# Optimization experiments

Measured on AMD Instinct MI355X. Metric: run time of the kernel, lower is better.

The kernel has to match this reference:

```python
import jax, jax.numpy as jnp
import numpy as np

B, N, E, H, A = 64, 64, 4032, 256, 4  # batch, max atoms, edges per mol, hidden, edge-attr dim
FI = 2 * H + 1 + A  # edge-MLP input dim = 517
SCALE = 15.0


def setup_inputs() -> dict:
    key = jax.random.key(0)
    ks = jax.random.split(key, 16)
    w = lambda k, s: jax.random.normal(k, s, jnp.float32) * 0.05
    # edge indices with i != j to avoid degenerate zero-distance edges
    ii = jax.random.randint(ks[3], (B, E), 0, N)
    off = jax.random.randint(ks[4], (B, E), 1, N)
    jj = (ii + off) % N
    edge_indices = jnp.stack([ii, jj], axis=-1).astype(jnp.int32)
    return dict(
        x=jax.random.normal(ks[0], (B, N, 3), jnp.float32),
        h=jax.random.normal(ks[1], (B, N, H), jnp.float32),
        a=jax.random.normal(ks[2], (B, E, A), jnp.float32),
        edge_indices=edge_indices,
        node_mask=jnp.ones((B, N, 1), jnp.float32),
        edge_mask=jnp.ones((B, E, 1), jnp.float32),
        We1=w(ks[5], (FI, 256)), be1=jnp.zeros(256, jnp.float32),
        We2=w(ks[6], (256, 256)), be2=jnp.zeros(256, jnp.float32),
        Wa=w(ks[7], (256, 1)), ba=jnp.zeros(1, jnp.float32),
        Wh1=w(ks[8], (H + 256, 256)), bh1=jnp.zeros(256, jnp.float32),
        Wh2=w(ks[9], (256, 256)), bh2=jnp.zeros(256, jnp.float32),
        Wx1=w(ks[10], (FI, 256)), bx1=jnp.zeros(256, jnp.float32),
        Wx2=w(ks[11], (256, 256)), bx2=jnp.zeros(256, jnp.float32),
        Wx3=w(ks[12], (256, 1)),
    )


def reference(x, h, a, edge_indices, node_mask, edge_mask,
              We1, be1, We2, be2, Wa, ba,
              Wh1, bh1, Wh2, bh2, Wx1, bx1, Wx2, bx2, Wx3):
    silu = jax.nn.silu
    bidx = jnp.arange(B)[:, None]                      # [B,1] batch gather index
    ii, jj = edge_indices[..., 0], edge_indices[..., 1]
    x_i, x_j = x[bidx, ii], x[bidx, jj]                # [B,E,3]
    diff = (x_i - x_j) * edge_mask                     # [B,E,3]
    d = jnp.sqrt(jnp.sum(diff * diff, -1, keepdims=True))  # [B,E,1]
    h_i, h_j = h[bidx, ii], h[bidx, jj]                # [B,E,H]
    feat = jnp.concatenate([h_i, h_j, d * d, a], -1)   # [B,E,517]
    # edge MLP + attention gate
    m = silu(silu(feat @ We1 + be1) @ We2 + be2)       # [B,E,256]
    e = jax.nn.sigmoid(m @ Wa + ba)                    # [B,E,1]
    em = e * m
    # scatter-add to source nodes (replaces the one-hot matmul, same math)
    seg = (bidx * N + ii).reshape(-1)                  # [B*E]
    em_agg = jax.ops.segment_sum(em.reshape(B * E, 256), seg,
                                 num_segments=B * N).reshape(B, N, 256)
    h_out = (h + silu(jnp.concatenate([h, em_agg], -1) @ Wh1 + bh1) @ Wh2 + bh2) * node_mask
    # coordinate update
    xw = jnp.tanh(silu(silu(feat @ Wx1 + bx1) @ Wx2 + bx2) @ Wx3) * SCALE  # [B,E,1]
    xm = xw * diff / (d + 1.0)                         # [B,E,3]
    x_agg = jax.ops.segment_sum(xm.reshape(B * E, 3), seg,
                                num_segments=B * N).reshape(B, N, 3)
    x_out = (x + x_agg) * node_mask
    return x_out, h_out
```

## Files before the change

kernel.cpp:

```cpp
#include <hip/hip_runtime.h>

#define E_ 4032
#define TE 64
#define NB 4032

typedef unsigned int uint;
typedef unsigned short ushort;
typedef __attribute__((ext_vector_type(8))) short short8;
typedef __attribute__((ext_vector_type(4))) float f32x4;
typedef __attribute__((ext_vector_type(2))) float f32x2;

__device__ __forceinline__ ushort f2bf(float x) {
  uint u = __float_as_uint(x);
  return (ushort)((u + 0x7fffu + ((u >> 16) & 1u)) >> 16);
}
__device__ __forceinline__ uint pack2(float lo, float hi) {
  return (uint)f2bf(lo) | ((uint)f2bf(hi) << 16);
}
__device__ __forceinline__ uint cvtpk(float lo, float hi) {
  uint r;
  asm("v_cvt_pk_bf16_f32 %0, %1, %2" : "=v"(r) : "v"(lo), "v"(hi));
  return r;
}
__device__ __forceinline__ float exp2_(float x) {
  float r;
  asm("v_exp_f32 %0, %1" : "=v"(r) : "v"(x));
  return r;
}
__device__ __forceinline__ float bflo(uint u) { return __uint_as_float(u << 16); }
__device__ __forceinline__ float bfhi(uint u) { return __uint_as_float(u & 0xffff0000u); }
__device__ __forceinline__ float bf2f(ushort s) { return __uint_as_float((uint)s << 16); }
__device__ __forceinline__ float rcp_(float x) { return __builtin_amdgcn_rcpf(x); }
__device__ __forceinline__ float silu_(float v) { return v * rcp_(1.0f + exp2_(v * -1.44269504f)); }
__device__ __forceinline__ float sigmoid_(float v) { return rcp_(1.0f + exp2_(v * -1.44269504f)); }
__device__ __forceinline__ float tanh_(float v) { return 1.0f - 2.0f * rcp_(1.0f + exp2_(v * 2.88539008f)); }

__device__ __forceinline__ f32x2 silu2(f32x2 v) {
  f32x2 nm = v * (f32x2){-1.44269504f, -1.44269504f};
  f32x2 e = {exp2_(nm.x), exp2_(nm.y)};
  f32x2 den = e + (f32x2){1.0f, 1.0f};
  f32x2 r = {rcp_(den.x), rcp_(den.y)};
  return v * r;
}

__device__ __forceinline__ void atom_pk_bf16(ushort* p, uint v) {
  asm volatile("global_atomic_pk_add_bf16 %0, %1, off" :: "v"(p), "v"(v) : "memory");
}

template <int RM>
__device__ __forceinline__ void gemmT(const ushort* Ab, const ushort* Bmat,
                                      int w, int l15, int lhi, f32x4 acc[RM][4]) {
#pragma unroll
  for (int ks = 0; ks < 8; ++ks) {
    short8 av[RM];
#pragma unroll
    for (int rm = 0; rm < RM; ++rm) {
      int row = rm * 16 + l15;
      int byt = (ks * 64 + lhi * 16) ^ ((row & 7) << 4);
      av[rm] = *(const short8*)((const char*)Ab + row * 512 + byt);
    }
#pragma unroll
    for (int cn = 0; cn < 4; ++cn) {
      int col = w * 64 + cn * 16 + l15;
      short8 bv = *(const short8*)(Bmat + col * 256 + ks * 32 + lhi * 8);
#pragma unroll
      for (int rm = 0; rm < RM; ++rm)
        acc[rm][cn] = __builtin_amdgcn_mfma_f32_16x16x32_bf16(av[rm], bv, acc[rm][cn], 0, 0, 0);
    }
  }
}

__global__ __launch_bounds__(256) void k_count(const int* __restrict__ eidx,
                                               uint* __restrict__ cnt) {
  int g = blockIdx.x * 256 + threadIdx.x;
  int b = g / E_;
  int i = eidx[(size_t)g * 2];
  atomicAdd(&cnt[b * 64 + i], 1u);
}

__global__ __launch_bounds__(256) void k_scan(const uint* __restrict__ cnt,
                                              uint* __restrict__ cursor) {
  __shared__ uint sw[4];
  int t = threadIdx.x;
  uint loc[16];
  uint tot = 0;
#pragma unroll
  for (int q = 0; q < 16; ++q) {
    loc[q] = cnt[t * 16 + q];
    tot += loc[q];
  }
  uint v = tot;
#pragma unroll
  for (int d = 1; d < 64; d <<= 1) {
    uint u = __shfl_up(v, d);
    if ((t & 63) >= d) v += u;
  }
  if ((t & 63) == 63) sw[t >> 6] = v;
  __syncthreads();
  uint woff = 0;
  int wv = t >> 6;
  if (wv > 0) woff += sw[0];
  if (wv > 1) woff += sw[1];
  if (wv > 2) woff += sw[2];
  uint run = woff + v - tot;
#pragma unroll
  for (int q = 0; q < 16; ++q) {
    cursor[t * 16 + q] = run;
    run += loc[q];
  }
}

__global__ __launch_bounds__(256) void k_fill(const int* __restrict__ eidx,
                                              uint* __restrict__ cursor,
                                              uint* __restrict__ perm) {
  int g = blockIdx.x * 256 + threadIdx.x;
  int b = g / E_;
  int i = eidx[(size_t)g * 2];
  uint slot = atomicAdd(&cursor[b * 64 + i], 1u);
  perm[slot] = (uint)g;
}

__global__ __launch_bounds__(256) void k_prep(
    const float* __restrict__ We1, const float* __restrict__ Wx1,
    const float* __restrict__ Wh1, const float* __restrict__ We2,
    const float* __restrict__ Wx2, const float* __restrict__ Wh2,
    ushort* __restrict__ WT) {
  __shared__ float tl[64][65];
  int blk = blockIdx.x;
  int m = blk >> 4, tile = blk & 15;
  int kt = (tile & 3) * 64, nt = (tile >> 2) * 64;
  const float* src;
  switch (m) {
    case 0: src = We1; break;
    case 1: src = We1 + 65536; break;
    case 2: src = Wx1; break;
    case 3: src = Wx1 + 65536; break;
    case 4: src = Wh1; break;
    case 5: src = We2; break;
    case 6: src = Wx2; break;
    case 7: src = Wh1 + 65536; break;
    default: src = Wh2; break;
  }
  int t = threadIdx.x;
  int c = t & 63, r4 = t >> 6;
#pragma unroll
  for (int rr = 0; rr < 64; rr += 4)
    tl[rr + r4][c] = src[(size_t)(kt + rr + r4) * 256 + nt + c];
  __syncthreads();
#pragma unroll
  for (int rr = 0; rr < 64; rr += 4)
    WT[(size_t)m * 65536 + (size_t)(nt + rr + r4) * 256 + kt + c] = f2bf(tl[c][rr + r4]);
}

__global__ __launch_bounds__(256, 2) void k_proj(const float* __restrict__ h,
                                                 const ushort* __restrict__ WT,
                                                 ushort* __restrict__ P) {
  __shared__ ushort Ab[128 * 256];
  int t = threadIdx.x;
  int rowbase = (blockIdx.x & 31) * 128;
  int g = blockIdx.x >> 5;
  {
    int c2 = t & 127, es = t >> 7;
#pragma unroll 4
    for (int it = 0; it < 64; ++it) {
      int row = it * 2 + es;
      float2 v = *(const float2*)(h + (size_t)(rowbase + row) * 256 + c2 * 2);
      *(uint*)((char*)Ab + row * 512 + ((c2 * 4) ^ ((row & 7) << 4))) = cvtpk(v.x, v.y);
    }
  }
  __syncthreads();
  int w = t >> 6, lane = t & 63, l15 = lane & 15, lhi = lane >> 4;
  f32x4 acc[8][4] = {};
  gemmT<8>(Ab, WT + g * 65536, w, l15, lhi, acc);
#pragma unroll
  for (int rm = 0; rm < 8; ++rm)
#pragma unroll
    for (int cn = 0; cn < 4; ++cn)
#pragma unroll
      for (int r = 0; r < 4; ++r) {
        int row = rowbase + rm * 16 + lhi * 4 + r;
        int col = w * 64 + cn * 16 + l15;
        P[(size_t)row * 1280 + g * 256 + col] = f2bf(acc[rm][cn][r]);
      }
}

__device__ __forceinline__ void buildT1(int t, const uint* __restrict__ Pu,
                                        const float* __restrict__ Wbig,
                                        const float* __restrict__ b1, int offI,
                                        ushort* Ab, const uint* s_ij,
                                        const float* s_d2, const float4* s_a4) {
  int c2 = t & 63, es = t >> 6;
  int c0 = c2 * 4;
  const float* Wr = Wbig + 512 * 256 + c0;
  f32x2 w5A = *(const f32x2*)(Wr);        f32x2 w5B = *(const f32x2*)(Wr + 2);
  f32x2 a0A = *(const f32x2*)(Wr + 256);  f32x2 a0B = *(const f32x2*)(Wr + 258);
  f32x2 a1A = *(const f32x2*)(Wr + 512);  f32x2 a1B = *(const f32x2*)(Wr + 514);
  f32x2 a2A = *(const f32x2*)(Wr + 768);  f32x2 a2B = *(const f32x2*)(Wr + 770);
  f32x2 a3A = *(const f32x2*)(Wr + 1024); f32x2 a3B = *(const f32x2*)(Wr + 1026);
  f32x2 bbA = *(const f32x2*)(b1 + c0);   f32x2 bbB = *(const f32x2*)(b1 + c0 + 2);
  int offJ = offI + 128;
#pragma unroll 2
  for (int it = 0; it < 16; ++it) {
    int e = it * 4 + es;
    uint ij = s_ij[e];
    uint i4 = ij & 0xffffu, j4 = ij >> 16;
    f32x2 d2v;
    d2v.x = s_d2[e];
    d2v.y = d2v.x;
    float4 av = s_a4[e];
    uint2 pi = *(const uint2*)(Pu + i4 * 640u + (uint)(offI + c2 * 2));
    uint2 pj = *(const uint2*)(Pu + j4 * 640u + (uint)(offJ + c2 * 2));
    f32x2 vA = (f32x2){bflo(pi.x), bfhi(pi.x)} + (f32x2){bflo(pj.x), bfhi(pj.x)};
    f32x2 vB = (f32x2){bflo(pi.y), bfhi(pi.y)} + (f32x2){bflo(pj.y), bfhi(pj.y)};
    f32x2 axv = {av.x, av.x}, ayv = {av.y, av.y}, azv = {av.z, av.z}, awv = {av.w, av.w};
    f32x2 zA = bbA + d2v * w5A + axv * a0A + ayv * a1A + azv * a2A + awv * a3A;
    f32x2 zB = bbB + d2v * w5B + axv * a0B + ayv * a1B + azv * a2B + awv * a3B;
    vA = silu2(vA + zA);
    vB = silu2(vB + zB);
    uint2 o;
    o.x = cvtpk(vA.x, vA.y);
    o.y = cvtpk(vB.x, vB.y);
    *(uint2*)((char*)Ab + e * 512 + ((c0 * 2) ^ ((e & 7) << 4))) = o;
  }
}

__global__ __launch_bounds__(256, 4) void k_edge(
    const float* __restrict__ x, const int* __restrict__ eidx,
    const float* __restrict__ a, const float* __restrict__ emask,
    const uint* __restrict__ perm,
    const ushort* __restrict__ P, const ushort* __restrict__ WT,
    const float* __restrict__ We1, const float* __restrict__ be1,
    const float* __restrict__ be2, const float* __restrict__ Wa,
    const float* __restrict__ ba,
    const float* __restrict__ Wx1, const float* __restrict__ bx1,
    const float* __restrict__ bx2, const float* __restrict__ Wx3,
    ushort* __restrict__ em_agg, float* __restrict__ x_agg) {
  __shared__ ushort Ab[TE * 256];
  __shared__ uint s_ij[TE];
  __shared__ float s_d2[TE];
  __shared__ float4 s_a4[TE];
  __shared__ float s_dx[TE], s_dy[TE], s_dz[TE];
  __shared__ float s_red[2][TE];
  __shared__ float s_gate[TE];
  __shared__ ushort s_seghead[TE + 2];
  __shared__ int s_nseg;
  int t = threadIdx.x;
  int bid = blockIdx.x;
  bid = (bid & 7) * 504 + (bid >> 3);
  int ebase = bid * TE;

  if (t < TE) {
    int eid = (int)perm[ebase + t];
    int b = ebase / E_;
    int2 ij = *(const int2*)(eidx + (size_t)eid * 2);
    uint i4 = (uint)(b * 64 + ij.x);
    uint j4 = (uint)(b * 64 + ij.y);
    s_ij[t] = i4 | (j4 << 16);
    float m = emask[eid];
    float dx = (x[i4 * 3 + 0] - x[j4 * 3 + 0]) * m;
    float dy = (x[i4 * 3 + 1] - x[j4 * 3 + 1]) * m;
    float dz = (x[i4 * 3 + 2] - x[j4 * 3 + 2]) * m;
    s_d2[t] = dx * dx + dy * dy + dz * dz;
    s_dx[t] = dx; s_dy[t] = dy; s_dz[t] = dz;
    s_a4[t] = *(const float4*)(a + (size_t)eid * 4);
    s_red[0][t] = 0.f;
    s_red[1][t] = 0.f;
    uint prev = __shfl_up(i4, 1);
    int flag = (t == 0) || (i4 != prev);
    unsigned long long mask = __ballot(flag);
    int rank = (int)__popcll(mask & ((1ull << t) - 1ull));
    if (flag) s_seghead[rank] = (ushort)t;
    if (t == 0) {
      int ns = (int)__popcll(mask);
      s_nseg = ns;
      s_seghead[ns] = TE;
    }
  }
  __syncthreads();

  const uint* Pu = (const uint*)P;
  int w = t >> 6, lane = t & 63, l15 = lane & 15, lhi = lane >> 4;
  float ba0 = ba[0];

  buildT1(t, Pu, Wx1, bx1, 256, Ab, s_ij, s_d2, s_a4);
  __syncthreads();
  {
    f32x4 acc1[4][4] = {};
    gemmT<4>(Ab, WT + 6 * 65536, w, l15, lhi, acc1);
    int colb = w * 64 + l15;
    f32x2 wvA = {Wx3[colb], Wx3[colb + 16]};
    f32x2 wvB = {Wx3[colb + 32], Wx3[colb + 48]};
    f32x2 b2A = {bx2[colb], bx2[colb + 16]};
    f32x2 b2B = {bx2[colb + 32], bx2[colb + 48]};
#pragma unroll
    for (int rm = 0; rm < 4; ++rm)
#pragma unroll
      for (int r = 0; r < 4; ++r) {
        f32x2 mA = silu2((f32x2){acc1[rm][0][r], acc1[rm][1][r]} + b2A);
        f32x2 mB = silu2((f32x2){acc1[rm][2][r], acc1[rm][3][r]} + b2B);
        f32x2 q = mA * wvA + mB * wvB;
        float p = q.x + q.y;
        p += __shfl_xor(p, 1);
        p += __shfl_xor(p, 2);
        p += __shfl_xor(p, 4);
        p += __shfl_xor(p, 8);
        if (l15 == 0) atomicAdd(&s_red[1][rm * 16 + lhi * 4 + r], p);
      }
  }
  __syncthreads();

  if (t < TE) {
    float fac = tanh_(s_red[1][t]) * 15.0f * rcp_(sqrtf(s_d2[t]) + 1.0f);
    s_dx[t] *= fac; s_dy[t] *= fac; s_dz[t] *= fac;
  }
  __syncthreads();
  {
    int ns = s_nseg;
    for (int s = t; s < ns; s += 256) {
      int st = s_seghead[s], en = s_seghead[s + 1];
      float sx = 0.f, sy = 0.f, sz = 0.f;
      for (int r = st; r < en; ++r) { sx += s_dx[r]; sy += s_dy[r]; sz += s_dz[r]; }
      uint i4 = s_ij[st] & 0xffffu;
      atomicAdd(x_agg + i4 * 3u + 0, sx);
      atomicAdd(x_agg + i4 * 3u + 1, sy);
      atomicAdd(x_agg + i4 * 3u + 2, sz);
    }
  }

  buildT1(t, Pu, We1, be1, 0, Ab, s_ij, s_d2, s_a4);
  __syncthreads();
  f32x4 acc0[4][4] = {};
  gemmT<4>(Ab, WT + 5 * 65536, w, l15, lhi, acc0);
  {
    int colb = w * 64 + l15;
    f32x2 wvA = {Wa[colb], Wa[colb + 16]};
    f32x2 wvB = {Wa[colb + 32], Wa[colb + 48]};
    f32x2 b2A = {be2[colb], be2[colb + 16]};
    f32x2 b2B = {be2[colb + 32], be2[colb + 48]};
#pragma unroll
    for (int rm = 0; rm < 4; ++rm)
#pragma unroll
      for (int r = 0; r < 4; ++r) {
        f32x2 mA = silu2((f32x2){acc0[rm][0][r], acc0[rm][1][r]} + b2A);
        f32x2 mB = silu2((f32x2){acc0[rm][2][r], acc0[rm][3][r]} + b2B);
        acc0[rm][0][r] = mA.x; acc0[rm][1][r] = mA.y;
        acc0[rm][2][r] = mB.x; acc0[rm][3][r] = mB.y;
        f32x2 q = mA * wvA + mB * wvB;
        float p = q.x + q.y;
        p += __shfl_xor(p, 1);
        p += __shfl_xor(p, 2);
        p += __shfl_xor(p, 4);
        p += __shfl_xor(p, 8);
        if (l15 == 0) atomicAdd(&s_red[0][rm * 16 + lhi * 4 + r], p);
      }
  }
  __syncthreads();

  if (t < TE) s_gate[t] = sigmoid_(s_red[0][t] + ba0);
  uint* AbU = (uint*)Ab;
#pragma unroll
  for (int rm = 0; rm < 4; ++rm)
#pragma unroll
    for (int r = 0; r < 4; ++r) {
      int row = rm * 16 + lhi * 4 + r;
#pragma unroll
      for (int cn = 0; cn < 4; ++cn) {
        float vme = acc0[rm][cn][r];
        float vpo = __shfl_xor(vme, 1);
        if (!(l15 & 1)) {
          int cp = (w * 64 + cn * 16 + l15) >> 1;
          AbU[row * 128 + cp] = cvtpk(vme, vpo);
        }
      }
    }
  __syncthreads();

  {
    int ns = s_nseg;
    int c = t & 127;
    for (int s = t >> 7; s < ns; s += 2) {
      int st = s_seghead[s], en = s_seghead[s + 1];
      f32x2 sum = {0.f, 0.f};
      for (int r = st; r < en; ++r) {
        uint u = AbU[r * 128 + c];
        f32x2 gv = {s_gate[r], s_gate[r]};
        sum += gv * (f32x2){bflo(u), bfhi(u)};
      }
      uint i4 = s_ij[st] & 0xffffu;
      atom_pk_bf16(em_agg + i4 * 256u + (uint)(c * 2), cvtpk(sum.x, sum.y));
    }
  }
}

__global__ __launch_bounds__(256, 2) void k_node(
    const float* __restrict__ h, const float* __restrict__ x,
    const float* __restrict__ nmask,
    const ushort* __restrict__ em_agg, const float* __restrict__ x_agg,
    const ushort* __restrict__ P, const ushort* __restrict__ WT,
    const float* __restrict__ bh1, const float* __restrict__ bh2,
    float* __restrict__ out) {
  __shared__ ushort Ab[64 * 256];
  int t = threadIdx.x;
  int rowbase = blockIdx.x * 64;
  {
    const uint* emu = (const uint*)em_agg;
    int c2 = t & 127, es = t >> 7;
#pragma unroll 4
    for (int it = 0; it < 32; ++it) {
      int row = it * 2 + es;
      uint v = emu[(size_t)(rowbase + row) * 128 + c2];
      *(uint*)((char*)Ab + row * 512 + ((c2 * 4) ^ ((row & 7) << 4))) = v;
    }
  }
  __syncthreads();
  int w = t >> 6, lane = t & 63, l15 = lane & 15, lhi = lane >> 4;
  {
    f32x4 acc[4][4] = {};
    gemmT<4>(Ab, WT + 7 * 65536, w, l15, lhi, acc);
    __syncthreads();
    float bc[4];
#pragma unroll
    for (int cn = 0; cn < 4; ++cn) bc[cn] = bh1[w * 64 + cn * 16 + l15];
#pragma unroll
    for (int rm = 0; rm < 4; ++rm)
#pragma unroll
      for (int cn = 0; cn < 4; ++cn)
#pragma unroll
        for (int r = 0; r < 4; ++r) {
          int row = rm * 16 + lhi * 4 + r;
          int col = w * 64 + cn * 16 + l15;
          float q1 = bf2f(P[(size_t)(rowbase + row) * 1280 + 1024 + col]);
          float sv = silu_(acc[rm][cn][r] + q1 + bc[cn]);
          *(ushort*)((char*)Ab + row * 512 + ((col * 2) ^ ((row & 7) << 4))) = f2bf(sv);
        }
  }
  __syncthreads();
  {
    f32x4 acc[4][4] = {};
    gemmT<4>(Ab, WT + 8 * 65536, w, l15, lhi, acc);
    float bc[4];
#pragma unroll
    for (int cn = 0; cn < 4; ++cn) bc[cn] = bh2[w * 64 + cn * 16 + l15];
#pragma unroll
    for (int rm = 0; rm < 4; ++rm)
#pragma unroll
      for (int cn = 0; cn < 4; ++cn)
#pragma unroll
        for (int r = 0; r < 4; ++r) {
          int row = rowbase + rm * 16 + lhi * 4 + r;
          int col = w * 64 + cn * 16 + l15;
          float o = (h[(size_t)row * 256 + col] + acc[rm][cn][r] + bc[cn]) * nmask[row];
          out[12288 + (size_t)row * 256 + col] = o;
        }
  }
  if (t < 64) {
    int row = rowbase + t;
    float nm = nmask[row];
#pragma unroll
    for (int c = 0; c < 3; ++c)
      out[row * 3 + c] = (x[row * 3 + c] + x_agg[row * 3 + c]) * nm;
  }
}

extern "C" void kernel_launch(void* const* d_in, const int* in_sizes, int n_in,
                              void* d_out, int out_size, void* d_ws, size_t ws_size,
                              hipStream_t stream) {
  (void)in_sizes; (void)n_in; (void)out_size; (void)ws_size;
  const float* x = (const float*)d_in[0];
  const float* h = (const float*)d_in[1];
  const float* a = (const float*)d_in[2];
  const int* eidx = (const int*)d_in[3];
  const float* nmask = (const float*)d_in[4];
  const float* emask = (const float*)d_in[5];
  const float* We1 = (const float*)d_in[6];
  const float* be1 = (const float*)d_in[7];
  const float* We2 = (const float*)d_in[8];
  const float* be2 = (const float*)d_in[9];
  const float* Wa = (const float*)d_in[10];
  const float* ba = (const float*)d_in[11];
  const float* Wh1 = (const float*)d_in[12];
  const float* bh1 = (const float*)d_in[13];
  const float* Wh2 = (const float*)d_in[14];
  const float* bh2 = (const float*)d_in[15];
  const float* Wx1 = (const float*)d_in[16];
  const float* bx1 = (const float*)d_in[17];
  const float* Wx2 = (const float*)d_in[18];
  const float* bx2 = (const float*)d_in[19];
  const float* Wx3 = (const float*)d_in[20];

  char* ws = (char*)d_ws;
  ushort* WT = (ushort*)ws;
  ushort* P = (ushort*)(ws + 1179648);
  ushort* em_agg = (ushort*)(ws + 11665408);
  float* x_agg = (float*)(ws + 13762560);
  uint* cnt = (uint*)(ws + 13811712);
  uint* cursor = (uint*)(ws + 13828096);
  uint* perm = (uint*)(ws + 13844480);

  hipMemsetAsync(em_agg, 0, 2097152 + 49152 + 16384, stream);
  k_count<<<1008, 256, 0, stream>>>(eidx, cnt);
  k_scan<<<1, 256, 0, stream>>>(cnt, cursor);
  k_fill<<<1008, 256, 0, stream>>>(eidx, cursor, perm);
  k_prep<<<144, 256, 0, stream>>>(We1, Wx1, Wh1, We2, Wx2, Wh2, WT);
  k_proj<<<160, 256, 0, stream>>>(h, WT, P);
  k_edge<<<NB, 256, 0, stream>>>(x, eidx, a, emask, perm, P, WT, We1, be1, be2, Wa, ba,
                                 Wx1, bx1, bx2, Wx3, em_agg, x_agg);
  k_node<<<64, 256, 0, stream>>>(h, x, nmask, em_agg, x_agg, P, WT, bh1, bh2,
                                 (float*)d_out);
}
```

Before: 289.7 us.

## Fuse setup kernels, restructure edge aggregation, and halve node-kernel tile

```diff
diff --git a/kernel.cpp b/kernel.cpp
--- a/kernel.cpp
+++ b/kernel.cpp
@@ -13,9 +13,6 @@
 __device__ __forceinline__ ushort f2bf(float x) {
   uint u = __float_as_uint(x);
   return (ushort)((u + 0x7fffu + ((u >> 16) & 1u)) >> 16);
-}
-__device__ __forceinline__ uint pack2(float lo, float hi) {
-  return (uint)f2bf(lo) | ((uint)f2bf(hi) << 16);
 }
 __device__ __forceinline__ uint cvtpk(float lo, float hi) {
   uint r;
@@ -52,6 +49,12 @@
                                       int w, int l15, int lhi, f32x4 acc[RM][4]) {
 #pragma unroll
   for (int ks = 0; ks < 8; ++ks) {
+    short8 bv[4];
+#pragma unroll
+    for (int cn = 0; cn < 4; ++cn) {
+      int col = w * 64 + cn * 16 + l15;
+      bv[cn] = *(const short8*)(Bmat + col * 256 + ks * 32 + lhi * 8);
+    }
     short8 av[RM];
 #pragma unroll
     for (int rm = 0; rm < RM; ++rm) {
@@ -60,73 +63,30 @@
       av[rm] = *(const short8*)((const char*)Ab + row * 512 + byt);
     }
 #pragma unroll
-    for (int cn = 0; cn < 4; ++cn) {
-      int col = w * 64 + cn * 16 + l15;
-      short8 bv = *(const short8*)(Bmat + col * 256 + ks * 32 + lhi * 8);
+    for (int cn = 0; cn < 4; ++cn)
 #pragma unroll
       for (int rm = 0; rm < RM; ++rm)
-        acc[rm][cn] = __builtin_amdgcn_mfma_f32_16x16x32_bf16(av[rm], bv, acc[rm][cn], 0, 0, 0);
-    }
-  }
-}
-
-__global__ __launch_bounds__(256) void k_count(const int* __restrict__ eidx,
-                                               uint* __restrict__ cnt) {
-  int g = blockIdx.x * 256 + threadIdx.x;
-  int b = g / E_;
-  int i = eidx[(size_t)g * 2];
-  atomicAdd(&cnt[b * 64 + i], 1u);
-}
-
-__global__ __launch_bounds__(256) void k_scan(const uint* __restrict__ cnt,
-                                              uint* __restrict__ cursor) {
-  __shared__ uint sw[4];
-  int t = threadIdx.x;
-  uint loc[16];
-  uint tot = 0;
-#pragma unroll
-  for (int q = 0; q < 16; ++q) {
-    loc[q] = cnt[t * 16 + q];
-    tot += loc[q];
-  }
-  uint v = tot;
-#pragma unroll
-  for (int d = 1; d < 64; d <<= 1) {
-    uint u = __shfl_up(v, d);
-    if ((t & 63) >= d) v += u;
-  }
-  if ((t & 63) == 63) sw[t >> 6] = v;
-  __syncthreads();
-  uint woff = 0;
-  int wv = t >> 6;
-  if (wv > 0) woff += sw[0];
-  if (wv > 1) woff += sw[1];
-  if (wv > 2) woff += sw[2];
-  uint run = woff + v - tot;
-#pragma unroll
-  for (int q = 0; q < 16; ++q) {
-    cursor[t * 16 + q] = run;
-    run += loc[q];
-  }
-}
-
-__global__ __launch_bounds__(256) void k_fill(const int* __restrict__ eidx,
-                                              uint* __restrict__ cursor,
-                                              uint* __restrict__ perm) {
-  int g = blockIdx.x * 256 + threadIdx.x;
-  int b = g / E_;
-  int i = eidx[(size_t)g * 2];
-  uint slot = atomicAdd(&cursor[b * 64 + i], 1u);
-  perm[slot] = (uint)g;
-}
-
-__global__ __launch_bounds__(256) void k_prep(
+        acc[rm][cn] = __builtin_amdgcn_mfma_f32_16x16x32_bf16(av[rm], bv[cn], acc[rm][cn], 0, 0, 0);
+  }
+}
+
+__global__ __launch_bounds__(256) void k_count_prep(
+    const int* __restrict__ eidx, uint* __restrict__ cnt,
     const float* __restrict__ We1, const float* __restrict__ Wx1,
     const float* __restrict__ Wh1, const float* __restrict__ We2,
     const float* __restrict__ Wx2, const float* __restrict__ Wh2,
     ushort* __restrict__ WT) {
   __shared__ float tl[64][65];
-  int blk = blockIdx.x;
+  int bid = blockIdx.x;
+  int t = threadIdx.x;
+  if (bid < 1008) {
+    int g = bid * 256 + t;
+    int b = g / E_;
+    int i = eidx[(size_t)g * 2];
+    atomicAdd(&cnt[b * 64 + i], 1u);
+    return;
+  }
+  int blk = bid - 1008;
   int m = blk >> 4, tile = blk & 15;
   int kt = (tile & 3) * 64, nt = (tile >> 2) * 64;
   const float* src;
@@ -141,7 +101,6 @@
     case 7: src = Wh1 + 65536; break;
     default: src = Wh2; break;
   }
-  int t = threadIdx.x;
   int c = t & 63, r4 = t >> 6;
 #pragma unroll
   for (int rr = 0; rr < 64; rr += 4)
@@ -152,13 +111,56 @@
     WT[(size_t)m * 65536 + (size_t)(nt + rr + r4) * 256 + kt + c] = f2bf(tl[c][rr + r4]);
 }
 
-__global__ __launch_bounds__(256, 2) void k_proj(const float* __restrict__ h,
-                                                 const ushort* __restrict__ WT,
-                                                 ushort* __restrict__ P) {
+__global__ __launch_bounds__(256) void k_scan(const uint* __restrict__ cnt,
+                                              uint* __restrict__ cursor) {
+  __shared__ uint sw[4];
+  int t = threadIdx.x;
+  uint loc[16];
+  uint tot = 0;
+#pragma unroll
+  for (int q = 0; q < 16; ++q) {
+    loc[q] = cnt[t * 16 + q];
+    tot += loc[q];
+  }
+  uint v = tot;
+#pragma unroll
+  for (int d = 1; d < 64; d <<= 1) {
+    uint u = __shfl_up(v, d);
+    if ((t & 63) >= d) v += u;
+  }
+  if ((t & 63) == 63) sw[t >> 6] = v;
+  __syncthreads();
+  uint woff = 0;
+  int wv = t >> 6;
+  if (wv > 0) woff += sw[0];
+  if (wv > 1) woff += sw[1];
+  if (wv > 2) woff += sw[2];
+  uint run = woff + v - tot;
+#pragma unroll
+  for (int q = 0; q < 16; ++q) {
+    cursor[t * 16 + q] = run;
+    run += loc[q];
+  }
+}
+
+__global__ __launch_bounds__(256, 2) void k_fill_proj(
+    const int* __restrict__ eidx, uint* __restrict__ cursor,
+    uint* __restrict__ perm, const float* __restrict__ h,
+    const ushort* __restrict__ WT, ushort* __restrict__ P) {
   __shared__ ushort Ab[128 * 256];
+  int bid = blockIdx.x;
   int t = threadIdx.x;
-  int rowbase = (blockIdx.x & 31) * 128;
-  int g = blockIdx.x >> 5;
+  if (bid < 1008) {
+    int g = bid * 256 + t;
+    int b = g / E_;
+    int i = eidx[(size_t)g * 2];
+    uint slot = atomicAdd(&cursor[b * 64 + i], 1u);
+    perm[slot] = (uint)g;
+    return;
+  }
+  int blk = bid - 1008;
+  int rowbase = (blk & 31) * 128;
+  int g = blk >> 5;
   {
     int c2 = t & 127, es = t >> 7;
 #pragma unroll 4
@@ -187,7 +189,8 @@
 __device__ __forceinline__ void buildT1(int t, const uint* __restrict__ Pu,
                                         const float* __restrict__ Wbig,
                                         const float* __restrict__ b1, int offI,
-                                        ushort* Ab, const uint* s_ij,
+                                        ushort* Ab, const uint* s_pio,
+                                        const uint* s_pjo,
                                         const float* s_d2, const float4* s_a4) {
   int c2 = t & 63, es = t >> 6;
   int c0 = c2 * 4;
@@ -198,18 +201,17 @@
   f32x2 a2A = *(const f32x2*)(Wr + 768);  f32x2 a2B = *(const f32x2*)(Wr + 770);
   f32x2 a3A = *(const f32x2*)(Wr + 1024); f32x2 a3B = *(const f32x2*)(Wr + 1026);
   f32x2 bbA = *(const f32x2*)(b1 + c0);   f32x2 bbB = *(const f32x2*)(b1 + c0 + 2);
-  int offJ = offI + 128;
-#pragma unroll 2
+  const uint* Pme = Pu + (uint)(offI + c2 * 2);
+  const uint* Pmj = Pu + (uint)(offI + 128 + c2 * 2);
+#pragma unroll
   for (int it = 0; it < 16; ++it) {
     int e = it * 4 + es;
-    uint ij = s_ij[e];
-    uint i4 = ij & 0xffffu, j4 = ij >> 16;
+    uint2 pi = *(const uint2*)(Pme + s_pio[e]);
+    uint2 pj = *(const uint2*)(Pmj + s_pjo[e]);
     f32x2 d2v;
     d2v.x = s_d2[e];
     d2v.y = d2v.x;
     float4 av = s_a4[e];
-    uint2 pi = *(const uint2*)(Pu + i4 * 640u + (uint)(offI + c2 * 2));
-    uint2 pj = *(const uint2*)(Pu + j4 * 640u + (uint)(offJ + c2 * 2));
     f32x2 vA = (f32x2){bflo(pi.x), bfhi(pi.x)} + (f32x2){bflo(pj.x), bfhi(pj.x)};
     f32x2 vB = (f32x2){bflo(pi.y), bfhi(pi.y)} + (f32x2){bflo(pj.y), bfhi(pj.y)};
     f32x2 axv = {av.x, av.x}, ayv = {av.y, av.y}, azv = {av.z, av.z}, awv = {av.w, av.w};
@@ -237,11 +239,11 @@
     ushort* __restrict__ em_agg, float* __restrict__ x_agg) {
   __shared__ ushort Ab[TE * 256];
   __shared__ uint s_ij[TE];
+  __shared__ uint s_pio[TE], s_pjo[TE];
   __shared__ float s_d2[TE];
   __shared__ float4 s_a4[TE];
   __shared__ float s_dx[TE], s_dy[TE], s_dz[TE];
   __shared__ float s_red[2][TE];
-  __shared__ float s_gate[TE];
   __shared__ ushort s_seghead[TE + 2];
   __shared__ int s_nseg;
   int t = threadIdx.x;
@@ -256,6 +258,8 @@
     uint i4 = (uint)(b * 64 + ij.x);
     uint j4 = (uint)(b * 64 + ij.y);
     s_ij[t] = i4 | (j4 << 16);
+    s_pio[t] = i4 * 640u;
+    s_pjo[t] = j4 * 640u;
     float m = emask[eid];
     float dx = (x[i4 * 3 + 0] - x[j4 * 3 + 0]) * m;
     float dy = (x[i4 * 3 + 1] - x[j4 * 3 + 1]) * m;
@@ -282,7 +286,7 @@
   int w = t >> 6, lane = t & 63, l15 = lane & 15, lhi = lane >> 4;
   float ba0 = ba[0];
 
-  buildT1(t, Pu, Wx1, bx1, 256, Ab, s_ij, s_d2, s_a4);
+  buildT1(t, Pu, Wx1, bx1, 256, Ab, s_pio, s_pjo, s_d2, s_a4);
   __syncthreads();
   {
     f32x4 acc1[4][4] = {};
@@ -309,26 +313,34 @@
   }
   __syncthreads();
 
-  if (t < TE) {
-    float fac = tanh_(s_red[1][t]) * 15.0f * rcp_(sqrtf(s_d2[t]) + 1.0f);
-    s_dx[t] *= fac; s_dy[t] *= fac; s_dz[t] *= fac;
-  }
-  __syncthreads();
+  buildT1(t, Pu, We1, be1, 0, Ab, s_pio, s_pjo, s_d2, s_a4);
+  __syncthreads();
+
   {
     int ns = s_nseg;
-    for (int s = t; s < ns; s += 256) {
+    for (int s = w; s < ns; s += 4) {
       int st = s_seghead[s], en = s_seghead[s + 1];
+      int r = st + lane;
       float sx = 0.f, sy = 0.f, sz = 0.f;
-      for (int r = st; r < en; ++r) { sx += s_dx[r]; sy += s_dy[r]; sz += s_dz[r]; }
-      uint i4 = s_ij[st] & 0xffffu;
-      atomicAdd(x_agg + i4 * 3u + 0, sx);
-      atomicAdd(x_agg + i4 * 3u + 1, sy);
-      atomicAdd(x_agg + i4 * 3u + 2, sz);
-    }
-  }
-
-  buildT1(t, Pu, We1, be1, 0, Ab, s_ij, s_d2, s_a4);
-  __syncthreads();
+      if (r < en) {
+        float fac = tanh_(s_red[1][r]) * 15.0f * rcp_(sqrtf(s_d2[r]) + 1.0f);
+        sx = fac * s_dx[r]; sy = fac * s_dy[r]; sz = fac * s_dz[r];
+      }
+#pragma unroll
+      for (int d = 1; d < 64; d <<= 1) {
+        sx += __shfl_xor(sx, d);
+        sy += __shfl_xor(sy, d);
+        sz += __shfl_xor(sz, d);
+      }
+      if (lane == 0) {
+        uint i4 = s_ij[st] & 0xffffu;
+        atomicAdd(x_agg + i4 * 3u + 0, sx);
+        atomicAdd(x_agg + i4 * 3u + 1, sy);
+        atomicAdd(x_agg + i4 * 3u + 2, sz);
+      }
+    }
+  }
+
   f32x4 acc0[4][4] = {};
   gemmT<4>(Ab, WT + 5 * 65536, w, l15, lhi, acc0);
   {
@@ -356,16 +368,16 @@
   }
   __syncthreads();
 
-  if (t < TE) s_gate[t] = sigmoid_(s_red[0][t] + ba0);
   uint* AbU = (uint*)Ab;
 #pragma unroll
   for (int rm = 0; rm < 4; ++rm)
 #pragma unroll
     for (int r = 0; r < 4; ++r) {
       int row = rm * 16 + lhi * 4 + r;
+      float g = sigmoid_(s_red[0][row] + ba0);
 #pragma unroll
       for (int cn = 0; cn < 4; ++cn) {
-        float vme = acc0[rm][cn][r];
+        float vme = g * acc0[rm][cn][r];
         float vpo = __shfl_xor(vme, 1);
         if (!(l15 & 1)) {
           int cp = (w * 64 + cn * 16 + l15) >> 1;
@@ -383,8 +395,7 @@
       f32x2 sum = {0.f, 0.f};
       for (int r = st; r < en; ++r) {
         uint u = AbU[r * 128 + c];
-        f32x2 gv = {s_gate[r], s_gate[r]};
-        sum += gv * (f32x2){bflo(u), bfhi(u)};
+        sum += (f32x2){bflo(u), bfhi(u)};
       }
       uint i4 = s_ij[st] & 0xffffu;
       atom_pk_bf16(em_agg + i4 * 256u + (uint)(c * 2), cvtpk(sum.x, sum.y));
@@ -399,14 +410,14 @@
     const ushort* __restrict__ P, const ushort* __restrict__ WT,
     const float* __restrict__ bh1, const float* __restrict__ bh2,
     float* __restrict__ out) {
-  __shared__ ushort Ab[64 * 256];
+  __shared__ ushort Ab[32 * 256];
   int t = threadIdx.x;
-  int rowbase = blockIdx.x * 64;
+  int rowbase = blockIdx.x * 32;
   {
     const uint* emu = (const uint*)em_agg;
     int c2 = t & 127, es = t >> 7;
 #pragma unroll 4
-    for (int it = 0; it < 32; ++it) {
+    for (int it = 0; it < 16; ++it) {
       int row = it * 2 + es;
       uint v = emu[(size_t)(rowbase + row) * 128 + c2];
       *(uint*)((char*)Ab + row * 512 + ((c2 * 4) ^ ((row & 7) << 4))) = v;
@@ -415,14 +426,14 @@
   __syncthreads();
   int w = t >> 6, lane = t & 63, l15 = lane & 15, lhi = lane >> 4;
   {
-    f32x4 acc[4][4] = {};
-    gemmT<4>(Ab, WT + 7 * 65536, w, l15, lhi, acc);
+    f32x4 acc[2][4] = {};
+    gemmT<2>(Ab, WT + 7 * 65536, w, l15, lhi, acc);
     __syncthreads();
     float bc[4];
 #pragma unroll
     for (int cn = 0; cn < 4; ++cn) bc[cn] = bh1[w * 64 + cn * 16 + l15];
 #pragma unroll
-    for (int rm = 0; rm < 4; ++rm)
+    for (int rm = 0; rm < 2; ++rm)
 #pragma unroll
       for (int cn = 0; cn < 4; ++cn)
 #pragma unroll
@@ -436,13 +447,13 @@
   }
   __syncthreads();
   {
-    f32x4 acc[4][4] = {};
-    gemmT<4>(Ab, WT + 8 * 65536, w, l15, lhi, acc);
+    f32x4 acc[2][4] = {};
+    gemmT<2>(Ab, WT + 8 * 65536, w, l15, lhi, acc);
     float bc[4];
 #pragma unroll
     for (int cn = 0; cn < 4; ++cn) bc[cn] = bh2[w * 64 + cn * 16 + l15];
 #pragma unroll
-    for (int rm = 0; rm < 4; ++rm)
+    for (int rm = 0; rm < 2; ++rm)
 #pragma unroll
       for (int cn = 0; cn < 4; ++cn)
 #pragma unroll
@@ -453,7 +464,7 @@
           out[12288 + (size_t)row * 256 + col] = o;
         }
   }
-  if (t < 64) {
+  if (t < 32) {
     int row = rowbase + t;
     float nm = nmask[row];
 #pragma unroll
@@ -498,13 +509,11 @@
   uint* perm = (uint*)(ws + 13844480);
 
   hipMemsetAsync(em_agg, 0, 2097152 + 49152 + 16384, stream);
-  k_count<<<1008, 256, 0, stream>>>(eidx, cnt);
+  k_count_prep<<<1152, 256, 0, stream>>>(eidx, cnt, We1, Wx1, Wh1, We2, Wx2, Wh2, WT);
   k_scan<<<1, 256, 0, stream>>>(cnt, cursor);
-  k_fill<<<1008, 256, 0, stream>>>(eidx, cursor, perm);
-  k_prep<<<144, 256, 0, stream>>>(We1, Wx1, Wh1, We2, Wx2, Wh2, WT);
-  k_proj<<<160, 256, 0, stream>>>(h, WT, P);
+  k_fill_proj<<<1168, 256, 0, stream>>>(eidx, cursor, perm, h, WT, P);
   k_edge<<<NB, 256, 0, stream>>>(x, eidx, a, emask, perm, P, WT, We1, be1, be2, Wa, ba,
                                  Wx1, bx1, bx2, Wx3, em_agg, x_agg);
-  k_node<<<64, 256, 0, stream>>>(h, x, nmask, em_agg, x_agg, P, WT, bh1, bh2,
-                                 (float*)d_out);
-}
+  k_node<<<128, 256, 0, stream>>>(h, x, nmask, em_agg, x_agg, P, WT, bh1, bh2,
+                                  (float*)d_out);
+}
```

After: 287.1 us. Within noise of the previous version (-0.9%).
